# Performance work log

Hardware: AMD Instinct MI355X
Metric: run time of the kernel (lower is better)

The kernel has to match this reference:

```python
import jax, jax.numpy as jnp
import numpy as np

N_EDGE_TYPES = 25
EF = 2  # edge feature dim (excluding type)
HID = 10


def _edge_nn(et, ef, emb, wh, bh, wg, bg):
    # y = relu(emb[et] * (ef@Wh+bh) + (ef@Wg+bg)) -> [E, in*out]
    return jax.nn.relu(emb[et] * (ef @ wh + bh) + (ef @ wg + bg))


def _nnconv(x, et, ef, src, dst, emb, wh, bh, wg, bg, root, bias, in_c, out_c):
    n = x.shape[0]
    w = _edge_nn(et, ef, emb, wh, bh, wg, bg).reshape(-1, in_c, out_c)  # [E,in,out]
    msg = jnp.einsum('ei,eio->eo', x[src], w)                          # per-edge matmul
    s = jax.ops.segment_sum(msg, dst, num_segments=n)
    cnt = jax.ops.segment_sum(jnp.ones((src.shape[0],), x.dtype), dst, num_segments=n)
    agg = s / jnp.maximum(cnt, 1.0)[:, None]                           # scatter-mean
    return agg + x @ root + bias


def _make_params(key, in_c, out_c):
    ks = jax.random.split(key, 6)
    d = in_c * out_c
    s = 0.1
    return dict(
        emb=jax.random.normal(ks[0], (N_EDGE_TYPES, d), jnp.float32) * s,
        wh=jax.random.normal(ks[1], (EF, d), jnp.float32) * s,
        bh=jax.random.normal(ks[2], (d,), jnp.float32) * s,
        wg=jax.random.normal(ks[3], (EF, d), jnp.float32) * s,
        bg=jax.random.normal(ks[4], (d,), jnp.float32) * s,
        root=jax.random.normal(ks[5], (in_c, out_c), jnp.float32) * s,
        bias=jnp.zeros((out_c,), jnp.float32),
    )


def setup_inputs() -> dict:
    key = jax.random.key(0)
    ks = jax.random.split(key, 12)
    N, E, IN_C, OUT_C, B = 50000, 250000, 16, 16, 8
    inp = {
        'x': jax.random.normal(ks[0], (N, IN_C), jnp.float32),
        'edge_feat': jax.random.normal(ks[1], (E, EF), jnp.float32),
        'edge_type': jax.random.randint(ks[2], (E,), 0, N_EDGE_TYPES),
        'edge_src': jax.random.randint(ks[3], (E,), 0, N),
        'edge_dst': jax.random.randint(ks[4], (E,), 0, N),
        'cell_type': jax.random.randint(ks[5], (N,), 0, 3),
        'batch_ids': jnp.sort(jax.random.randint(ks[6], (N,), 0, B)),
        'batch_size': B,
    }
    for i, (ic, oc) in enumerate([(IN_C, HID), (HID, HID), (HID, OUT_C)], start=1):
        p = _make_params(ks[6 + i], ic, oc)
        for k, v in p.items():
            inp[f'{k}{i}'] = v
    return inp


def reference(x, edge_feat,
              emb1, wh1, bh1, wg1, bg1, root1, bias1,
              emb2, wh2, bh2, wg2, bg2, root2, bias2,
              emb3, wh3, bh3, wg3, bg3, root3, bias3,
              edge_type, edge_src, edge_dst, cell_type, batch_ids, batch_size):
    in_c, out_c = x.shape[1], root3.shape[1]
    h = _nnconv(x, edge_type, edge_feat, edge_src, edge_dst,
                emb1, wh1, bh1, wg1, bg1, root1, bias1, in_c, HID)
    h = jax.nn.relu(h)  # dropout is identity in eval mode
    h = _nnconv(h, edge_type, edge_feat, edge_src, edge_dst,
                emb2, wh2, bh2, wg2, bg2, root2, bias2, HID, HID)
    h = jax.nn.relu(h)
    h = _nnconv(h, edge_type, edge_feat, edge_src, edge_dst,
                emb3, wh3, bh3, wg3, bg3, root3, bias3, HID, out_c)
    h = jax.nn.relu(h)
    # scatter-mean pooling over nodes with cell_type==1, grouped by graph id
    gate = (cell_type == 1).astype(jnp.int32)
    idx = gate * (batch_ids.astype(jnp.int32) + 1)  # 0 = discarded bucket
    nseg = batch_size + 1
    s = jax.ops.segment_sum(h, idx, num_segments=nseg)
    cnt = jax.ops.segment_sum(jnp.ones((h.shape[0],), h.dtype), idx, num_segments=nseg)
    pooled = s / jnp.maximum(cnt, 1.0)[:, None]
    return pooled[1:batch_size + 1, :]  # [B, out_c]
```

## Files before the change

### kernel.cpp

```cpp
#include <hip/hip_runtime.h>
#include <stdint.h>

#define IN1 16
#define HIDC 10
#define OUT3 16
#define NTYPES 25
#define MAXB 8
#define HSTR 12

#define D1 (IN1 * HIDC)
#define D2 (HIDC * HIDC)
#define D3 (HIDC * OUT3)

__global__ __launch_bounds__(256) void init_kernel(
    const float* __restrict__ emb1, const float* __restrict__ wh1,
    const float* __restrict__ bh1, const float* __restrict__ wg1,
    const float* __restrict__ bg1,
    const float* __restrict__ emb2, const float* __restrict__ wh2,
    const float* __restrict__ bh2, const float* __restrict__ wg2,
    const float* __restrict__ bg2,
    const float* __restrict__ emb3, const float* __restrict__ wh3,
    const float* __restrict__ bh3, const float* __restrict__ wg3,
    const float* __restrict__ bg3,
    float4* __restrict__ P1, float4* __restrict__ P2, float4* __restrict__ P3,
    int* __restrict__ deg, int N,
    float* __restrict__ psum, float* __restrict__ pcnt, int B)
{
  int gtid = blockIdx.x * 256 + threadIdx.x;
  int gstr = gridDim.x * 256;
  const int nPrep = NTYPES * (D1 + D2 + D3);
  for (int i = gtid; i < nPrep; i += gstr) {
    const float *emb, *wh, *bh, *wg, *bg; float4* P; int D, k;
    if (i < NTYPES * D1) {
      emb = emb1; wh = wh1; bh = bh1; wg = wg1; bg = bg1; P = P1; D = D1; k = i;
    } else if (i < NTYPES * (D1 + D2)) {
      emb = emb2; wh = wh2; bh = bh2; wg = wg2; bg = bg2; P = P2; D = D2;
      k = i - NTYPES * D1;
    } else {
      emb = emb3; wh = wh3; bh = bh3; wg = wg3; bg = bg3; P = P3; D = D3;
      k = i - NTYPES * (D1 + D2);
    }
    int j = k - (k / D) * D;
    float e = emb[k];
    float4 p;
    p.x = fmaf(e, wh[j],     wg[j]);
    p.y = fmaf(e, wh[D + j], wg[D + j]);
    p.z = fmaf(e, bh[j],     bg[j]);
    p.w = 0.f;
    P[k] = p;
  }
  for (int i = gtid; i < N; i += gstr) deg[i] = 0;
  for (int i = gtid; i < B * 16; i += gstr) psum[i] = 0.f;
  for (int i = gtid; i < B; i += gstr) pcnt[i] = 0.f;
}

__global__ __launch_bounds__(256) void hist_kernel(const int* __restrict__ edst,
                                                   int* __restrict__ deg,
                                                   int* __restrict__ pos, int E) {
  int e = blockIdx.x * blockDim.x + threadIdx.x;
  if (e < E) pos[e] = atomicAdd(&deg[edst[e]], 1);
}

__global__ __launch_bounds__(256) void scan_part_kernel(const int* __restrict__ deg,
                                                        int* __restrict__ row_ptr,
                                                        int* __restrict__ bsum, int N) {
  __shared__ int wsums[4];
  int tid = threadIdx.x, lane = tid & 63, wid = tid >> 6;
  int idx0 = (blockIdx.x * 256 + tid) * 4;
  int4 v = make_int4(0, 0, 0, 0);
  if (idx0 < N)     v.x = deg[idx0];
  if (idx0 + 1 < N) v.y = deg[idx0 + 1];
  if (idx0 + 2 < N) v.z = deg[idx0 + 2];
  if (idx0 + 3 < N) v.w = deg[idx0 + 3];
  int s = v.x + v.y + v.z + v.w;
  int x = s;
  #pragma unroll
  for (int off = 1; off < 64; off <<= 1) {
    int y = __shfl_up(x, off);
    if (lane >= off) x += y;
  }
  if (lane == 63) wsums[wid] = x;
  __syncthreads();
  int wpre = 0;
  #pragma unroll
  for (int w = 0; w < 4; ++w) if (w < wid) wpre += wsums[w];
  int excl = x - s + wpre;
  if (idx0 < N)     row_ptr[idx0]     = excl;
  if (idx0 + 1 < N) row_ptr[idx0 + 1] = excl + v.x;
  if (idx0 + 2 < N) row_ptr[idx0 + 2] = excl + v.x + v.y;
  if (idx0 + 3 < N) row_ptr[idx0 + 3] = excl + v.x + v.y + v.z;
  if (tid == 255) bsum[blockIdx.x] = excl + s;
}

__global__ __launch_bounds__(256) void scan_add2_kernel(int* __restrict__ row_ptr,
                                                        const int* __restrict__ bsum,
                                                        int N, int chunks) {
  __shared__ int s_off;
  int c = blockIdx.x, tid = threadIdx.x;
  if (tid < 64) {
    int v = (tid < c) ? bsum[tid] : 0;
    #pragma unroll
    for (int off = 32; off >= 1; off >>= 1) v += __shfl_xor(v, off);
    if (tid == 0) s_off = v;
  }
  __syncthreads();
  int off = s_off;
  int base = c * 1024 + tid * 4;
  #pragma unroll
  for (int j = 0; j < 4; ++j) {
    int idx = base + j;
    if (idx < N) row_ptr[idx] += off;
  }
  if (c == chunks - 1 && tid == 0) row_ptr[N] = off + bsum[c];
}

__global__ __launch_bounds__(256) void permute_kernel(
    const int* __restrict__ edst, const int* __restrict__ esrc,
    const int* __restrict__ et, const float2* __restrict__ ef,
    const int* __restrict__ row_ptr, const int* __restrict__ pos,
    int4* __restrict__ edges, int E) {
  int e = blockIdx.x * blockDim.x + threadIdx.x;
  if (e >= E) return;
  int d = edst[e];
  int idx = row_ptr[d] + pos[e];
  float2 f = ef[e];
  int4 r;
  r.x = esrc[e];
  r.y = et[e];
  r.z = __float_as_int(f.x);
  r.w = __float_as_int(f.y);
  edges[idx] = r;
}

template<int IN_C, int O, int XS, bool POOL, int BS>
__global__ __launch_bounds__(BS) void layer_kernel(
    const float* __restrict__ xin, const int4* __restrict__ edges,
    const int* __restrict__ row_ptr, const float4* __restrict__ Pg,
    const float* __restrict__ root, const float* __restrict__ bias,
    float* __restrict__ hout, const int* __restrict__ ctype,
    const int* __restrict__ bids, float* __restrict__ pcnt, int N, int B)
{
  constexpr int D = IN_C * O;
  constexpr int TSTR = D + 1;
  constexpr int NPW = 4;
  constexpr int NPB = (BS / 64) * NPW;
  __shared__ float4 s_P[NTYPES * TSTR];
  __shared__ float s_psum[POOL ? (MAXB * 16) : 1];
  __shared__ float s_pcnt[POOL ? MAXB : 1];

  int tid = threadIdx.x;
  for (int k = tid; k < NTYPES * D; k += BS) {
    int t = k / D, j = k - t * D;
    s_P[t * TSTR + j] = Pg[k];
  }
  if (POOL) {
    for (int i = tid; i < MAXB * 16; i += BS) s_psum[i] = 0.f;
    for (int i = tid; i < MAXB; i += BS) s_pcnt[i] = 0.f;
  }
  __syncthreads();

  int lane = tid & 63;
  int wv = tid >> 6;
  int o = lane & 15;
  int es = lane >> 4;
  int oc = (O == 16) ? o : ((o < O) ? o : 0);
  int nb = (blockIdx.x * (BS / 64) + wv) * NPW;

  float accs = 0.f;
  int degs = 0;

  #pragma unroll
  for (int s = 0; s < NPW; ++s) {
    int n = nb + s;
    float acc = 0.f;
    int start = 0, end = 0;
    if (n < N) { start = row_ptr[n]; end = row_ptr[n + 1]; }
    for (int e = start + es; e < end; e += 4) {
      int4 r = edges[e];
      float f0 = __int_as_float(r.z), f1 = __int_as_float(r.w);
      const float4* __restrict__ pb = s_P + r.y * TSTR + oc;
      const float* __restrict__ xr = xin + (size_t)r.x * XS;
      #pragma unroll
      for (int q = 0; q < IN_C / 4; ++q) {
        float4 xq = ((const float4*)xr)[q];
        float4 p0 = pb[(4 * q + 0) * O];
        float4 p1 = pb[(4 * q + 1) * O];
        float4 p2 = pb[(4 * q + 2) * O];
        float4 p3 = pb[(4 * q + 3) * O];
        acc = fmaf(xq.x, fmaxf(fmaf(f0, p0.x, fmaf(f1, p0.y, p0.z)), 0.f), acc);
        acc = fmaf(xq.y, fmaxf(fmaf(f0, p1.x, fmaf(f1, p1.y, p1.z)), 0.f), acc);
        acc = fmaf(xq.z, fmaxf(fmaf(f0, p2.x, fmaf(f1, p2.y, p2.z)), 0.f), acc);
        acc = fmaf(xq.w, fmaxf(fmaf(f0, p3.x, fmaf(f1, p3.y, p3.z)), 0.f), acc);
      }
      if constexpr (IN_C % 4 == 2) {
        float2 xq = ((const float2*)xr)[IN_C / 2 - 1];
        float4 p0 = pb[(IN_C - 2) * O];
        float4 p1 = pb[(IN_C - 1) * O];
        acc = fmaf(xq.x, fmaxf(fmaf(f0, p0.x, fmaf(f1, p0.y, p0.z)), 0.f), acc);
        acc = fmaf(xq.y, fmaxf(fmaf(f0, p1.x, fmaf(f1, p1.y, p1.z)), 0.f), acc);
      }
    }
    acc += __shfl_xor(acc, 16);
    acc += __shfl_xor(acc, 32);
    if (es == s) { accs = acc; degs = end - start; }
  }

  int n = nb + es;
  if (n < N && o < O) {
    float inv = 1.0f / fmaxf((float)degs, 1.0f);
    float v = fmaf(accs, inv, bias[o]);
    const float* __restrict__ xr = xin + (size_t)n * XS;
    #pragma unroll
    for (int i = 0; i < IN_C; ++i) v = fmaf(xr[i], root[i * O + o], v);
    v = fmaxf(v, 0.f);
    if (!POOL) {
      hout[(size_t)n * HSTR + o] = v;
    } else {
      if (ctype[n] == 1) {
        int b = bids[n];
        atomicAdd(&s_psum[b * 16 + o], v);
        if (o == 0) atomicAdd(&s_pcnt[b], 1.0f);
      }
    }
  }

  if (POOL) {
    __syncthreads();
    for (int i = tid; i < B * 16; i += BS) {
      float v = s_psum[i];
      if (v != 0.f) atomicAdd(&hout[i], v);
    }
    for (int i = tid; i < B; i += BS) {
      float c = s_pcnt[i];
      if (c != 0.f) atomicAdd(&pcnt[i], c);
    }
  }
}

__global__ __launch_bounds__(256) void finalize_kernel(
    const float* __restrict__ psum, const float* __restrict__ pcnt,
    float* __restrict__ out, int B) {
  int i = blockIdx.x * blockDim.x + threadIdx.x;
  if (i >= B * OUT3) return;
  int b = i / OUT3;
  out[i] = psum[i] / fmaxf(pcnt[b], 1.0f);
}

extern "C" void kernel_launch(void* const* d_in, const int* in_sizes, int n_in,
                              void* d_out, int out_size, void* d_ws, size_t ws_size,
                              hipStream_t stream)
{
  const float* x     = (const float*)d_in[0];
  const float* ef    = (const float*)d_in[1];
  const int*   et    = (const int*)d_in[2];
  const int*   esrc  = (const int*)d_in[3];
  const int*   edst  = (const int*)d_in[4];
  const int*   ctype = (const int*)d_in[5];
  const int*   bids  = (const int*)d_in[6];
  const float* emb1 = (const float*)d_in[8];
  const float* wh1  = (const float*)d_in[9];
  const float* bh1  = (const float*)d_in[10];
  const float* wg1  = (const float*)d_in[11];
  const float* bg1  = (const float*)d_in[12];
  const float* root1= (const float*)d_in[13];
  const float* bias1= (const float*)d_in[14];
  const float* emb2 = (const float*)d_in[15];
  const float* wh2  = (const float*)d_in[16];
  const float* bh2  = (const float*)d_in[17];
  const float* wg2  = (const float*)d_in[18];
  const float* bg2  = (const float*)d_in[19];
  const float* root2= (const float*)d_in[20];
  const float* bias2= (const float*)d_in[21];
  const float* emb3 = (const float*)d_in[22];
  const float* wh3  = (const float*)d_in[23];
  const float* bh3  = (const float*)d_in[24];
  const float* wg3  = (const float*)d_in[25];
  const float* bg3  = (const float*)d_in[26];
  const float* root3= (const float*)d_in[27];
  const float* bias3= (const float*)d_in[28];

  const int N = in_sizes[0] / IN1;
  const int E = in_sizes[2];
  const int B = out_size / OUT3;

  int4* edges   = (int4*)d_ws;
  int*  deg     = (int*)(edges + E);
  int*  pos     = deg + N;
  int*  row_ptr = pos + E;
  int*  bsum    = row_ptr + (N + 1);
  uintptr_t pp  = ((uintptr_t)(bsum + 64) + 15) & ~(uintptr_t)15;
  float4* P1    = (float4*)pp;
  float4* P2    = P1 + NTYPES * D1;
  float4* P3    = P2 + NTYPES * D2;
  float* h1     = (float*)(P3 + NTYPES * D3);
  float* h2     = h1 + (size_t)N * HSTR;
  float* psum   = h2 + (size_t)N * HSTR;
  float* pcnt   = psum + (size_t)B * 16;

  const int nChunk = (N + 1023) / 1024;

  init_kernel<<<128, 256, 0, stream>>>(
      emb1, wh1, bh1, wg1, bg1, emb2, wh2, bh2, wg2, bg2,
      emb3, wh3, bh3, wg3, bg3, P1, P2, P3, deg, N, psum, pcnt, B);
  hist_kernel<<<(E + 255) / 256, 256, 0, stream>>>(edst, deg, pos, E);
  scan_part_kernel<<<nChunk, 256, 0, stream>>>(deg, row_ptr, bsum, N);
  scan_add2_kernel<<<nChunk, 256, 0, stream>>>(row_ptr, bsum, N, nChunk);
  permute_kernel<<<(E + 255) / 256, 256, 0, stream>>>(
      edst, esrc, et, (const float2*)ef, row_ptr, pos, edges, E);

  const int g512 = (N + 31) / 32;
  layer_kernel<IN1, HIDC, IN1, false, 512><<<g512, 512, 0, stream>>>(
      x, edges, row_ptr, P1, root1, bias1,
      h1, nullptr, nullptr, nullptr, N, B);
  layer_kernel<HIDC, HIDC, HSTR, false, 512><<<g512, 512, 0, stream>>>(
      h1, edges, row_ptr, P2, root2, bias2,
      h2, nullptr, nullptr, nullptr, N, B);

  const int g1024 = (N + 63) / 64;
  layer_kernel<HIDC, OUT3, HSTR, true, 1024><<<g1024, 1024, 0, stream>>>(
      h2, edges, row_ptr, P3, root3, bias3,
      psum, ctype, bids, pcnt, N, B);

  finalize_kernel<<<1, 256, 0, stream>>>(psum, pcnt, (float*)d_out, B);
}
```

Measured before the change: 252.3 us.

## Split each layer into type-sorted edge message pass and CSR node reduction

Edges are bucketed by edge type into 32-edge padded chunks, so each wavefront keeps its type's edge-network coefficients in registers and skips the per-block shared-memory staging of all type tables. Each edge's message is written to a buffer indexed by its CSR position, and a second kernel per layer sums messages per destination node and applies root, bias and ReLU. This trades a much larger workspace, extra global writes and reads of per-edge messages, and twice the kernel launches for cheaper per-edge arithmetic. The old fused path is kept as a fallback when the workspace is too small.

Measured after the change: 258.0 us. +2.3%, slower.

```diff
diff --git a/kernel.cpp b/kernel.cpp
--- a/kernel.cpp
+++ b/kernel.cpp
@@ -7,6 +7,8 @@
 #define NTYPES 25
 #define MAXB 8
 #define HSTR 12
+#define MSTR 16
+#define CHUNK 32
 
 #define D1 (IN1 * HIDC)
 #define D2 (HIDC * HIDC)
@@ -24,7 +26,9 @@
     const float* __restrict__ bg3,
     float4* __restrict__ P1, float4* __restrict__ P2, float4* __restrict__ P3,
     int* __restrict__ deg, int N,
-    float* __restrict__ psum, float* __restrict__ pcnt, int B)
+    float* __restrict__ psum, float* __restrict__ pcnt,
+    int* __restrict__ thist,
+    int4* __restrict__ te, int* __restrict__ ci, int EPAD, int newpath, int B)
 {
   int gtid = blockIdx.x * 256 + threadIdx.x;
   int gstr = gridDim.x * 256;
@@ -52,13 +56,38 @@
   for (int i = gtid; i < N; i += gstr) deg[i] = 0;
   for (int i = gtid; i < B * 16; i += gstr) psum[i] = 0.f;
   for (int i = gtid; i < B; i += gstr) pcnt[i] = 0.f;
-}
-
-__global__ __launch_bounds__(256) void hist_kernel(const int* __restrict__ edst,
-                                                   int* __restrict__ deg,
-                                                   int* __restrict__ pos, int E) {
-  int e = blockIdx.x * blockDim.x + threadIdx.x;
-  if (e < E) pos[e] = atomicAdd(&deg[edst[e]], 1);
+  if (gtid < NTYPES) thist[gtid] = 0;
+  if (newpath) {
+    for (int i = gtid; i < EPAD; i += gstr) {
+      te[i] = make_int4(0, 0, 0, 0);
+      ci[i] = -1;
+    }
+  }
+}
+
+__global__ __launch_bounds__(256) void hist_kernel(
+    const int* __restrict__ edst, const int* __restrict__ et,
+    int* __restrict__ deg, int* __restrict__ pos,
+    int* __restrict__ thist, int* __restrict__ tpos, int E) {
+  __shared__ int s_cnt[NTYPES];
+  __shared__ int s_base[NTYPES];
+  int tid = threadIdx.x;
+  if (tid < NTYPES) s_cnt[tid] = 0;
+  __syncthreads();
+  int e = blockIdx.x * 256 + tid;
+  int t = 0, lr = 0, p = 0;
+  if (e < E) {
+    p = atomicAdd(&deg[edst[e]], 1);
+    t = et[e];
+    lr = atomicAdd(&s_cnt[t], 1);
+  }
+  __syncthreads();
+  if (tid < NTYPES && s_cnt[tid] > 0) s_base[tid] = atomicAdd(&thist[tid], s_cnt[tid]);
+  __syncthreads();
+  if (e < E) {
+    pos[e] = p;
+    tpos[e] = s_base[t] + lr;
+  }
 }
 
 __global__ __launch_bounds__(256) void scan_part_kernel(const int* __restrict__ deg,
@@ -94,6 +123,8 @@
 
 __global__ __launch_bounds__(256) void scan_add2_kernel(int* __restrict__ row_ptr,
                                                         const int* __restrict__ bsum,
+                                                        const int* __restrict__ thist,
+                                                        int* __restrict__ toff,
                                                         int N, int chunks) {
   __shared__ int s_off;
   int c = blockIdx.x, tid = threadIdx.x;
@@ -103,6 +134,18 @@
     for (int off = 32; off >= 1; off >>= 1) v += __shfl_xor(v, off);
     if (tid == 0) s_off = v;
   }
+  if (c == 0 && tid >= 64 && tid < 128) {
+    int l = tid - 64;
+    int b = (l < NTYPES) ? ((thist[l] + CHUNK - 1) & ~(CHUNK - 1)) : 0;
+    int x = b;
+    #pragma unroll
+    for (int off = 1; off < 32; off <<= 1) {
+      int y = __shfl_up(x, off);
+      if (l >= off) x += y;
+    }
+    if (l < NTYPES) toff[l] = x - b;
+    if (l == NTYPES - 1) toff[NTYPES] = x;
+  }
   __syncthreads();
   int off = s_off;
   int base = c * 1024 + tid * 4;
@@ -114,6 +157,21 @@
   if (c == chunks - 1 && tid == 0) row_ptr[N] = off + bsum[c];
 }
 
+__global__ __launch_bounds__(256) void permuteT_kernel(
+    const int* __restrict__ edst, const int* __restrict__ esrc,
+    const int* __restrict__ et, const float2* __restrict__ ef,
+    const int* __restrict__ row_ptr, const int* __restrict__ pos,
+    const int* __restrict__ tpos, const int* __restrict__ toff,
+    int4* __restrict__ te, int* __restrict__ ci, int E) {
+  int e = blockIdx.x * blockDim.x + threadIdx.x;
+  if (e >= E) return;
+  int t = et[e];
+  int slot = toff[t] + tpos[e];
+  float2 f = ef[e];
+  te[slot] = make_int4(esrc[e], t, __float_as_int(f.x), __float_as_int(f.y));
+  ci[slot] = row_ptr[edst[e]] + pos[e];
+}
+
 __global__ __launch_bounds__(256) void permute_kernel(
     const int* __restrict__ edst, const int* __restrict__ esrc,
     const int* __restrict__ et, const float2* __restrict__ ef,
@@ -121,15 +179,116 @@
     int4* __restrict__ edges, int E) {
   int e = blockIdx.x * blockDim.x + threadIdx.x;
   if (e >= E) return;
-  int d = edst[e];
-  int idx = row_ptr[d] + pos[e];
+  int idx = row_ptr[edst[e]] + pos[e];
   float2 f = ef[e];
-  int4 r;
-  r.x = esrc[e];
-  r.y = et[e];
-  r.z = __float_as_int(f.x);
-  r.w = __float_as_int(f.y);
-  edges[idx] = r;
+  edges[idx] = make_int4(esrc[e], et[e], __float_as_int(f.x), __float_as_int(f.y));
+}
+
+template<int IN_C, int O, int XS>
+__global__ __launch_bounds__(256) void edgeA_kernel(
+    const float* __restrict__ xin,
+    const int4* __restrict__ te,
+    const int* __restrict__ ci,
+    const float4* __restrict__ Pg,
+    float* __restrict__ msg,
+    const int* __restrict__ toff)
+{
+  int tid = threadIdx.x;
+  int lane = tid & 63;
+  int wv = blockIdx.x * 4 + (tid >> 6);
+  int base = wv * CHUNK;
+  if (base >= toff[NTYPES]) return;
+  int oc = lane & 15;
+  int es = lane >> 4;
+  int ocl = (O == 16) ? oc : ((oc < O) ? oc : 0);
+  int t = te[base].y;
+  float c0[IN_C], c1[IN_C], c2[IN_C];
+  const float4* __restrict__ pb = Pg + t * (IN_C * O) + ocl;
+  #pragma unroll
+  for (int i = 0; i < IN_C; ++i) {
+    float4 p = pb[i * O];
+    c0[i] = p.x; c1[i] = p.y; c2[i] = p.z;
+  }
+  #pragma unroll 1
+  for (int it = 0; it < CHUNK / 4; ++it) {
+    int slot = base + it * 4 + es;
+    int4 r = te[slot];
+    int cidx = ci[slot];
+    float f0 = __int_as_float(r.z), f1 = __int_as_float(r.w);
+    const float* __restrict__ xr = xin + (size_t)(unsigned)r.x * XS;
+    float acc = 0.f;
+    #pragma unroll
+    for (int q = 0; q < IN_C / 4; ++q) {
+      float4 xq = ((const float4*)xr)[q];
+      int i0 = 4 * q;
+      acc = fmaf(xq.x, fmaxf(fmaf(f0, c0[i0+0], fmaf(f1, c1[i0+0], c2[i0+0])), 0.f), acc);
+      acc = fmaf(xq.y, fmaxf(fmaf(f0, c0[i0+1], fmaf(f1, c1[i0+1], c2[i0+1])), 0.f), acc);
+      acc = fmaf(xq.z, fmaxf(fmaf(f0, c0[i0+2], fmaf(f1, c1[i0+2], c2[i0+2])), 0.f), acc);
+      acc = fmaf(xq.w, fmaxf(fmaf(f0, c0[i0+3], fmaf(f1, c1[i0+3], c2[i0+3])), 0.f), acc);
+    }
+    if constexpr (IN_C % 4 == 2) {
+      float2 xq = ((const float2*)xr)[IN_C / 2 - 1];
+      acc = fmaf(xq.x, fmaxf(fmaf(f0, c0[IN_C-2], fmaf(f1, c1[IN_C-2], c2[IN_C-2])), 0.f), acc);
+      acc = fmaf(xq.y, fmaxf(fmaf(f0, c0[IN_C-1], fmaf(f1, c1[IN_C-1], c2[IN_C-1])), 0.f), acc);
+    }
+    if (cidx >= 0 && oc < O) msg[(size_t)cidx * MSTR + oc] = acc;
+  }
+}
+
+template<int IN_C, int O, int XS, bool POOL, int BS>
+__global__ __launch_bounds__(BS) void nodeB_kernel(
+    const float* __restrict__ xin,
+    const float* __restrict__ msg,
+    const int* __restrict__ row_ptr,
+    const float* __restrict__ root, const float* __restrict__ bias,
+    float* __restrict__ hout, const int* __restrict__ ctype,
+    const int* __restrict__ bids, float* __restrict__ pcnt, int N, int B)
+{
+  constexpr int NPB = BS / 16;
+  __shared__ float s_psum[POOL ? (MAXB * 16) : 1];
+  __shared__ float s_pcnt[POOL ? MAXB : 1];
+  int tid = threadIdx.x;
+  if (POOL) {
+    for (int i = tid; i < MAXB * 16; i += BS) s_psum[i] = 0.f;
+    for (int i = tid; i < MAXB; i += BS) s_pcnt[i] = 0.f;
+    __syncthreads();
+  }
+  int nl = tid >> 4;
+  int o = tid & 15;
+  int n = blockIdx.x * NPB + nl;
+  float acc = 0.f;
+  int start = 0, end = 0;
+  if (n < N) { start = row_ptr[n]; end = row_ptr[n + 1]; }
+  for (int e = start; e < end; ++e) acc += msg[(size_t)e * MSTR + o];
+
+  if (n < N && o < O) {
+    float inv = 1.0f / fmaxf((float)(end - start), 1.0f);
+    float v = fmaf(acc, inv, bias[o]);
+    const float* __restrict__ xr = xin + (size_t)n * XS;
+    #pragma unroll
+    for (int i = 0; i < IN_C; ++i) v = fmaf(xr[i], root[i * O + o], v);
+    v = fmaxf(v, 0.f);
+    if (!POOL) {
+      hout[(size_t)n * HSTR + o] = v;
+    } else {
+      if (ctype[n] == 1) {
+        int b = bids[n];
+        atomicAdd(&s_psum[b * 16 + o], v);
+        if (o == 0) atomicAdd(&s_pcnt[b], 1.0f);
+      }
+    }
+  }
+  if (POOL) {
+    __syncthreads();
+    for (int i = tid; i < B * 16; i += BS) {
+      float v = s_psum[i];
+      if (v != 0.f) atomicAdd(&hout[i], v);
+    }
+    for (int i = tid; i < B; i += BS) {
+      float c = s_pcnt[i];
+      if (c != 0.f) atomicAdd(&pcnt[i], c);
+    }
+  }
 }
 
 template<int IN_C, int O, int XS, bool POOL, int BS>
@@ -143,11 +302,9 @@
   constexpr int D = IN_C * O;
   constexpr int TSTR = D + 1;
   constexpr int NPW = 4;
-  constexpr int NPB = (BS / 64) * NPW;
   __shared__ float4 s_P[NTYPES * TSTR];
   __shared__ float s_psum[POOL ? (MAXB * 16) : 1];
   __shared__ float s_pcnt[POOL ? MAXB : 1];
-
   int tid = threadIdx.x;
   for (int k = tid; k < NTYPES * D; k += BS) {
     int t = k / D, j = k - t * D;
@@ -158,17 +315,14 @@
     for (int i = tid; i < MAXB; i += BS) s_pcnt[i] = 0.f;
   }
   __syncthreads();
-
   int lane = tid & 63;
   int wv = tid >> 6;
   int o = lane & 15;
   int es = lane >> 4;
   int oc = (O == 16) ? o : ((o < O) ? o : 0);
   int nb = (blockIdx.x * (BS / 64) + wv) * NPW;
-
   float accs = 0.f;
   int degs = 0;
-
   #pragma unroll
   for (int s = 0; s < NPW; ++s) {
     int n = nb + s;
@@ -204,7 +358,6 @@
     acc += __shfl_xor(acc, 32);
     if (es == s) { accs = acc; degs = end - start; }
   }
-
   int n = nb + es;
   if (n < N && o < O) {
     float inv = 1.0f / fmaxf((float)degs, 1.0f);
@@ -223,7 +376,6 @@
       }
     }
   }
-
   if (POOL) {
     __syncthreads();
     for (int i = tid; i < B * 16; i += BS) {
@@ -282,13 +434,16 @@
   const int N = in_sizes[0] / IN1;
   const int E = in_sizes[2];
   const int B = out_size / OUT3;
-
-  int4* edges   = (int4*)d_ws;
-  int*  deg     = (int*)(edges + E);
-  int*  pos     = deg + N;
-  int*  row_ptr = pos + E;
+  const int EPAD = E + NTYPES * CHUNK;
+
+  int4* te      = (int4*)d_ws;
+  int*  ci      = (int*)(te + EPAD);
+  int*  deg     = ci + EPAD;
+  int*  row_ptr = deg + N;
   int*  bsum    = row_ptr + (N + 1);
-  uintptr_t pp  = ((uintptr_t)(bsum + 64) + 15) & ~(uintptr_t)15;
+  int*  thist   = bsum + 64;
+  int*  toff    = thist + 32;
+  uintptr_t pp  = ((uintptr_t)(toff + 32) + 15) & ~(uintptr_t)15;
   float4* P1    = (float4*)pp;
   float4* P2    = P1 + NTYPES * D1;
   float4* P3    = P2 + NTYPES * D2;
@@ -296,30 +451,52 @@
   float* h2     = h1 + (size_t)N * HSTR;
   float* psum   = h2 + (size_t)N * HSTR;
   float* pcnt   = psum + (size_t)B * 16;
+  uintptr_t mp  = ((uintptr_t)(pcnt + B) + 15) & ~(uintptr_t)15;
+  int*  pos     = (int*)mp;
+  int*  tpos    = pos + E;
+  float* msg    = (float*)mp;
+
+  size_t req_new = (mp - (uintptr_t)d_ws) + (size_t)E * MSTR * 4;
+  const bool newpath = (req_new <= ws_size);
 
   const int nChunk = (N + 1023) / 1024;
 
-  init_kernel<<<128, 256, 0, stream>>>(
+  init_kernel<<<512, 256, 0, stream>>>(
       emb1, wh1, bh1, wg1, bg1, emb2, wh2, bh2, wg2, bg2,
-      emb3, wh3, bh3, wg3, bg3, P1, P2, P3, deg, N, psum, pcnt, B);
-  hist_kernel<<<(E + 255) / 256, 256, 0, stream>>>(edst, deg, pos, E);
+      emb3, wh3, bh3, wg3, bg3, P1, P2, P3, deg, N, psum, pcnt,
+      thist, te, ci, EPAD, newpath ? 1 : 0, B);
+  hist_kernel<<<(E + 255) / 256, 256, 0, stream>>>(edst, et, deg, pos, thist, tpos, E);
   scan_part_kernel<<<nChunk, 256, 0, stream>>>(deg, row_ptr, bsum, N);
-  scan_add2_kernel<<<nChunk, 256, 0, stream>>>(row_ptr, bsum, N, nChunk);
-  permute_kernel<<<(E + 255) / 256, 256, 0, stream>>>(
-      edst, esrc, et, (const float2*)ef, row_ptr, pos, edges, E);
-
-  const int g512 = (N + 31) / 32;
-  layer_kernel<IN1, HIDC, IN1, false, 512><<<g512, 512, 0, stream>>>(
-      x, edges, row_ptr, P1, root1, bias1,
-      h1, nullptr, nullptr, nullptr, N, B);
-  layer_kernel<HIDC, HIDC, HSTR, false, 512><<<g512, 512, 0, stream>>>(
-      h1, edges, row_ptr, P2, root2, bias2,
-      h2, nullptr, nullptr, nullptr, N, B);
-
-  const int g1024 = (N + 63) / 64;
-  layer_kernel<HIDC, OUT3, HSTR, true, 1024><<<g1024, 1024, 0, stream>>>(
-      h2, edges, row_ptr, P3, root3, bias3,
-      psum, ctype, bids, pcnt, N, B);
+  scan_add2_kernel<<<nChunk, 256, 0, stream>>>(row_ptr, bsum, thist, toff, N, nChunk);
+
+  if (newpath) {
+    permuteT_kernel<<<(E + 255) / 256, 256, 0, stream>>>(
+        edst, esrc, et, (const float2*)ef, row_ptr, pos, tpos, toff, te, ci, E);
+
+    const int gA = ((EPAD + CHUNK - 1) / CHUNK + 3) / 4;
+    const int gB = (N + 15) / 16;
+    edgeA_kernel<IN1, HIDC, IN1><<<gA, 256, 0, stream>>>(x, te, ci, P1, msg, toff);
+    nodeB_kernel<IN1, HIDC, IN1, false, 256><<<gB, 256, 0, stream>>>(
+        x, msg, row_ptr, root1, bias1, h1, nullptr, nullptr, nullptr, N, B);
+    edgeA_kernel<HIDC, HIDC, HSTR><<<gA, 256, 0, stream>>>(h1, te, ci, P2, msg, toff);
+    nodeB_kernel<HIDC, HIDC, HSTR, false, 256><<<gB, 256, 0, stream>>>(
+        h1, msg, row_ptr, root2, bias2, h2, nullptr, nullptr, nullptr, N, B);
+    edgeA_kernel<HIDC, OUT3, HSTR><<<gA, 256, 0, stream>>>(h2, te, ci, P3, msg, toff);
+    const int gB3 = (N + 63) / 64;
+    nodeB_kernel<HIDC, OUT3, HSTR, true, 1024><<<gB3, 1024, 0, stream>>>(
+        h2, msg, row_ptr, root3, bias3, psum, ctype, bids, pcnt, N, B);
+  } else {
+    permute_kernel<<<(E + 255) / 256, 256, 0, stream>>>(
+        edst, esrc, et, (const float2*)ef, row_ptr, pos, te, E);
+    const int g512 = (N + 31) / 32;
+    layer_kernel<IN1, HIDC, IN1, false, 512><<<g512, 512, 0, stream>>>(
+        x, te, row_ptr, P1, root1, bias1, h1, nullptr, nullptr, nullptr, N, B);
+    layer_kernel<HIDC, HIDC, HSTR, false, 512><<<g512, 512, 0, stream>>>(
+        h1, te, row_ptr, P2, root2, bias2, h2, nullptr, nullptr, nullptr, N, B);
+    const int g1024 = (N + 63) / 64;
+    layer_kernel<HIDC, OUT3, HSTR, true, 1024><<<g1024, 1024, 0, stream>>>(
+        h2, te, row_ptr, P3, root3, bias3, psum, ctype, bids, pcnt, N, B);
+  }
 
   finalize_kernel<<<1, 256, 0, stream>>>(psum, pcnt, (float*)d_out, B);
 }
```
